# Performance work log

Hardware: AMD Instinct MI355X
Metric: run time of the kernel (lower is better)

The kernel has to match this reference:

```python
import jax, jax.numpy as jnp
import numpy as np

# Each of the 16 binary logic ops (probabilistic relaxation) is affine in (1, a, b, a*b):
# op(a,b) = c0 + ca*a + cb*b + cab*a*b. Rows indexed by op id 0..15.
COEF = jnp.array([
    [0, 0, 0, 0],   # 0: false
    [0, 0, 0, 1],   # 1: a AND b
    [0, 1, 0, -1],  # 2: a AND NOT b
    [0, 1, 0, 0],   # 3: a
    [0, 0, 1, -1],  # 4: NOT a AND b
    [0, 0, 1, 0],   # 5: b
    [0, 1, 1, -2],  # 6: a XOR b
    [0, 1, 1, -1],  # 7: a OR b
    [1, -1, -1, 1], # 8: NOR
    [1, -1, -1, 2], # 9: XNOR
    [1, 0, -1, 0],  # 10: NOT b
    [1, 0, -1, 1],  # 11: a OR NOT b
    [1, -1, 0, 0],  # 12: NOT a
    [1, -1, 0, 1],  # 13: NOT a OR b
    [1, 0, 0, -1],  # 14: NAND
    [1, 0, 0, 0],   # 15: true
], dtype=jnp.float32)

B, C, H, W = 64, 32, 32, 32
K = 64            # num_kernels
D = 4             # tree_depth
S = 2 ** D        # sample_size = 16
RF, STRIDE, PAD = 5, 1, 0


def _make_indices(rng):
    # Replicates get_kernel_indices: per-kernel random (h,w,c) offsets, tiled over all
    # spatial positions. Returns a_idx, b_idx: [K, P, S, 3] with (h, w, c).
    h_starts = np.arange(0, H + 2 * PAD - RF + 1, STRIDE)
    w_starts = np.arange(0, W + 2 * PAD - RF + 1, STRIDE)
    hg, wg = np.meshgrid(h_starts, w_starts, indexing='ij')
    hg, wg = hg.ravel(), wg.ravel()           # [P]
    a_all, b_all = [], []
    for _ in range(K):
        h_off = rng.integers(0, RF, 2 * S)
        w_off = rng.integers(0, RF, 2 * S)
        c_off = rng.integers(0, C, 2 * S)
        hh = h_off[None, :] + hg[:, None]     # [P, 2S]
        ww = w_off[None, :] + wg[:, None]
        cc = np.broadcast_to(c_off[None, :], hh.shape)
        idx = np.stack([hh, ww, cc], axis=-1) # [P, 2S, 3]
        a_all.append(idx[:, :S])
        b_all.append(idx[:, S:])
    return np.stack(a_all).astype(np.int32), np.stack(b_all).astype(np.int32)


def setup_inputs() -> dict:
    key = jax.random.key(0)
    kx, k0, k1, k2, k3, k4 = jax.random.split(key, 6)
    rng = np.random.default_rng(0)
    a_idx, b_idx = _make_indices(rng)
    return {
        'x': jax.random.uniform(kx, (B, C, H, W), dtype=jnp.float32),
        'w0': jax.random.normal(k0, (16, K, 16), dtype=jnp.float32),
        'w1': jax.random.normal(k1, (8, K, 16), dtype=jnp.float32),
        'w2': jax.random.normal(k2, (4, K, 16), dtype=jnp.float32),
        'w3': jax.random.normal(k3, (2, K, 16), dtype=jnp.float32),
        'w4': jax.random.normal(k4, (1, K, 16), dtype=jnp.float32),
        'a_idx': jnp.asarray(a_idx),
        'b_idx': jnp.asarray(b_idx),
    }


def _bin_op(a, b, w):
    # a, b: [B, K, P, L]; w: [L, K, 16] raw logits (softmaxed per original).
    p = jax.nn.softmax(w, axis=-1)                 # [L, K, 16]
    coef = jnp.einsum('lko,oc->ckl', p, COEF)      # [4, K, L]
    c = coef[:, None, :, None, :]                  # [4, 1, K, 1, L]
    return c[0] + c[1] * a + c[2] * b + c[3] * (a * b)


def reference(x, w0, w1, w2, w3, w4, a_idx, b_idx):
    ah, aw, ac = a_idx[..., 0], a_idx[..., 1], a_idx[..., 2]
    bh, bw, bc = b_idx[..., 0], b_idx[..., 1], b_idx[..., 2]
    a = x[:, ac, ah, aw]    # [B, K, P, S]
    b = x[:, bc, bh, bw]
    cur = _bin_op(a, b, w0)
    for w in (w1, w2, w3, w4):
        cur = _bin_op(cur[..., 0::2], cur[..., 1::2], w)
    return cur              # [B, K, P, 1]
```

## Files before the change

kernel.cpp:

```cpp
#include <hip/hip_runtime.h>
#include <hip/hip_bf16.h>


#define B_  64
#define C_  32
#define H_  32
#define W_  32
#define K_  64
#define P_  784
#define CHW (C_*H_*W_)
#define HW  (H_*W_)
#define SITES (K_*P_)
#define NPAIR (P_/2)

__constant__ float COEF_[16][4] = {
    {0, 0, 0, 0}, {0, 0, 0, 1}, {0, 1, 0, -1}, {0, 1, 0, 0},
    {0, 0, 1, -1}, {0, 0, 1, 0}, {0, 1, 1, -2}, {0, 1, 1, -1},
    {1, -1, -1, 1}, {1, -1, -1, 2}, {1, 0, -1, 0}, {1, 0, -1, 1},
    {1, -1, 0, 0}, {1, -1, 0, 1}, {1, 0, 0, -1}, {1, 0, 0, 0}
};

__global__ __launch_bounds__(256) void prep_kernel(
    const int* __restrict__ a_idx, const int* __restrict__ b_idx,
    const float* __restrict__ w0, const float* __restrict__ w1,
    const float* __restrict__ w2, const float* __restrict__ w3,
    const float* __restrict__ w4,
    int* __restrict__ baseAB,
    float4* __restrict__ cws)
{
    const int t = blockIdx.x * 256 + threadIdx.x;
    if (t < K_ * 32) {
        const int k = t >> 5;
        const int j = t & 31;
        const int* src = (j < 16) ? a_idx : b_idx;
        const int l = j & 15;
        const size_t ii = ((size_t)k * P_ * 16 + l) * 3;
        const int h = src[ii + 0];
        const int w = src[ii + 1];
        const int c = src[ii + 2];
        baseAB[t] = (c << 12) + (h << 7) + (w << 2);
    } else if (t < K_ * 32 + K_ * 31) {
        const int tt = t - K_ * 32;
        const int k = tt / 31;
        const int node = tt - k * 31;
        int d, l;
        if      (node < 16) { d = 0; l = node; }
        else if (node < 24) { d = 1; l = node - 16; }
        else if (node < 28) { d = 2; l = node - 24; }
        else if (node < 30) { d = 3; l = node - 28; }
        else                { d = 4; l = 0; }
        const float* W;
        switch (d) {
            case 0: W = w0; break;
            case 1: W = w1; break;
            case 2: W = w2; break;
            case 3: W = w3; break;
            default: W = w4; break;
        }
        const float* row = W + ((size_t)l * K_ + k) * 16;
        float m = row[0];
        #pragma unroll
        for (int o = 1; o < 16; ++o) m = fmaxf(m, row[o]);
        float e[16];
        float Z = 0.0f;
        #pragma unroll
        for (int o = 0; o < 16; ++o) { e[o] = expf(row[o] - m); Z += e[o]; }
        const float inv = 1.0f / Z;
        float c0 = 0.f, c1 = 0.f, c2 = 0.f, c3 = 0.f;
        #pragma unroll
        for (int o = 0; o < 16; ++o) {
            c0 += e[o] * COEF_[o][0];
            c1 += e[o] * COEF_[o][1];
            c2 += e[o] * COEF_[o][2];
            c3 += e[o] * COEF_[o][3];
        }
        cws[tt] = make_float4(c0 * inv, c1 * inv, c2 * inv, c3 * inv);
    }
}

__device__ __forceinline__ float binop(float a, float b, float4 c) {
    return fmaf(b, fmaf(c.w, a, c.z), fmaf(c.y, a, c.x));
}

__global__ __launch_bounds__(1024, 4) void logicconv_main(
    const float* __restrict__ x,
    const int* __restrict__ baseAB,
    const float4* __restrict__ cws,
    float* __restrict__ out)
{
    __shared__ float simg[CHW];

    const int tid = threadIdx.x;
    const int kg  = blockIdx.x >> 5;
    const int bp  = blockIdx.x & 31;
    const int b0  = bp * 2;

    {
        const float4* xi = (const float4*)(x + (size_t)b0 * CHW);
        float4* si = (float4*)simg;
        #pragma unroll
        for (int j = 0; j < 8; ++j)
            si[tid + j * 1024] = xi[tid + j * 1024];
    }
    __syncthreads();

    const int g    = __builtin_amdgcn_readfirstlane(tid >> 7);
    const int lane = tid & 127;
    const int k    = kg * 8 + g;

    const int*    __restrict__ bA = baseAB + k * 32;
    const float4* __restrict__ cw = cws + (size_t)k * 31;
    const char*   sb = (const char*)simg;
    const char*   x1 = (const char*)(x + (size_t)(b0 + 1) * CHW);
    float* __restrict__ o0 = out + ((size_t)b0 * K_ + k) * P_;
    float* __restrict__ o1 = o0 + (size_t)K_ * P_;

    for (int s = 0; s < 4; ++s) {
        const int t = s * 128 + lane;
        if (t < NPAIR) {
            const unsigned row  = (unsigned)t / 14u;
            const unsigned disp = 8u * (unsigned)t + 16u * row;

            float2 ye[16], yo[16];
            #pragma unroll
            for (int h = 0; h < 2; ++h) {
                unsigned ea[8], eb[8];
                #pragma unroll
                for (int j = 0; j < 8; ++j) {
                    ea[j] = (unsigned)bA[h*8 + j]      + disp;
                    eb[j] = (unsigned)bA[16 + h*8 + j] + disp;
                }
                float od[32];
                #pragma unroll
                for (int j = 0; j < 8; ++j) {
                    od[4*j+0] = *(const float*)(x1 + ea[j]);
                    od[4*j+1] = *(const float*)(x1 + ea[j] + 4);
                    od[4*j+2] = *(const float*)(x1 + eb[j]);
                    od[4*j+3] = *(const float*)(x1 + eb[j] + 4);
                }
                float ev[32];
                #pragma unroll
                for (int j = 0; j < 8; ++j) {
                    ev[4*j+0] = *(const float*)(sb + ea[j]);
                    ev[4*j+1] = *(const float*)(sb + ea[j] + 4);
                    ev[4*j+2] = *(const float*)(sb + eb[j]);
                    ev[4*j+3] = *(const float*)(sb + eb[j] + 4);
                }
                #pragma unroll
                for (int j = 0; j < 8; ++j) {
                    const int l = h*8 + j;
                    const float4 c = cw[l];
                    ye[l].x = binop(ev[4*j+0], ev[4*j+2], c);
                    ye[l].y = binop(ev[4*j+1], ev[4*j+3], c);
                    yo[l].x = binop(od[4*j+0], od[4*j+2], c);
                    yo[l].y = binop(od[4*j+1], od[4*j+3], c);
                }
            }
            #pragma unroll
            for (int l = 0; l < 8; ++l) {
                const float4 c = cw[16 + l];
                ye[l].x = binop(ye[2*l].x, ye[2*l+1].x, c);
                ye[l].y = binop(ye[2*l].y, ye[2*l+1].y, c);
                yo[l].x = binop(yo[2*l].x, yo[2*l+1].x, c);
                yo[l].y = binop(yo[2*l].y, yo[2*l+1].y, c);
            }
            #pragma unroll
            for (int l = 0; l < 4; ++l) {
                const float4 c = cw[24 + l];
                ye[l].x = binop(ye[2*l].x, ye[2*l+1].x, c);
                ye[l].y = binop(ye[2*l].y, ye[2*l+1].y, c);
                yo[l].x = binop(yo[2*l].x, yo[2*l+1].x, c);
                yo[l].y = binop(yo[2*l].y, yo[2*l+1].y, c);
            }
            #pragma unroll
            for (int l = 0; l < 2; ++l) {
                const float4 c = cw[28 + l];
                ye[l].x = binop(ye[2*l].x, ye[2*l+1].x, c);
                ye[l].y = binop(ye[2*l].y, ye[2*l+1].y, c);
                yo[l].x = binop(yo[2*l].x, yo[2*l+1].x, c);
                yo[l].y = binop(yo[2*l].y, yo[2*l+1].y, c);
            }
            {
                const float4 c = cw[30];
                float2 re, ro;
                re.x = binop(ye[0].x, ye[1].x, c);
                re.y = binop(ye[0].y, ye[1].y, c);
                ro.x = binop(yo[0].x, yo[1].x, c);
                ro.y = binop(yo[0].y, yo[1].y, c);
                *(float2*)(o0 + 2 * t) = re;
                *(float2*)(o1 + 2 * t) = ro;
            }
        }
    }
}

extern "C" void kernel_launch(void* const* d_in, const int* in_sizes, int n_in,
                              void* d_out, int out_size, void* d_ws, size_t ws_size,
                              hipStream_t stream) {
    const float* x     = (const float*)d_in[0];
    const float* w0    = (const float*)d_in[1];
    const float* w1    = (const float*)d_in[2];
    const float* w2    = (const float*)d_in[3];
    const float* w3    = (const float*)d_in[4];
    const float* w4    = (const float*)d_in[5];
    const int*   a_idx = (const int*)d_in[6];
    const int*   b_idx = (const int*)d_in[7];
    float* out = (float*)d_out;

    int*    baseAB = (int*)d_ws;
    float4* cws    = (float4*)((char*)d_ws + (size_t)K_ * 32 * 4);

    prep_kernel<<<16, 256, 0, stream>>>(a_idx, b_idx, w0, w1, w2, w3, w4,
                                        baseAB, cws);

    logicconv_main<<<256, 1024, 0, stream>>>(x, baseAB, cws, out);
}
```

Baseline: 30.15 us.

## Split shared image into even/odd columns and route some leaves to global

Stores the staged even-batch image in LDS de-interleaved into even-column and odd-column halves, with per-leaf precomputed base offsets and deltas. Each lane's stride-2 pixel pairs then map to consecutive LDS words, which aims to reduce bank conflicts. Only the first 14 leaves read from LDS. The last two leaves read directly from global memory, shifting some load from LDS onto the cache. This adds 56 registers of precomputed offsets, which may raise register pressure under the 1024-thread launch bound.

```diff
diff --git a/kernel.cpp b/kernel.cpp
--- a/kernel.cpp
+++ b/kernel.cpp
@@ -12,6 +12,7 @@
 #define HW  (H_*W_)
 #define SITES (K_*P_)
 #define NPAIR (P_/2)
+#define NLDS 14
 
 __constant__ float COEF_[16][4] = {
     {0, 0, 0, 0}, {0, 0, 0, 1}, {0, 1, 0, -1}, {0, 1, 0, 0},
@@ -97,10 +98,15 @@
 
     {
         const float4* xi = (const float4*)(x + (size_t)b0 * CHW);
-        float4* si = (float4*)simg;
-        #pragma unroll
-        for (int j = 0; j < 8; ++j)
-            si[tid + j * 1024] = xi[tid + j * 1024];
+        float2* se = (float2*)simg;
+        float2* so = ((float2*)simg) + 8192;
+        #pragma unroll
+        for (int j = 0; j < 8; ++j) {
+            const int u = tid + j * 1024;
+            const float4 v = xi[u];
+            se[u] = make_float2(v.x, v.z);
+            so[u] = make_float2(v.y, v.w);
+        }
     }
     __syncthreads();
 
@@ -110,45 +116,71 @@
 
     const int*    __restrict__ bA = baseAB + k * 32;
     const float4* __restrict__ cw = cws + (size_t)k * 31;
-    const char*   sb = (const char*)simg;
-    const char*   x1 = (const char*)(x + (size_t)(b0 + 1) * CHW);
+
+    int sB[2 * NLDS], sD[2 * NLDS];
+    #pragma unroll
+    for (int j = 0; j < NLDS; ++j) {
+        #pragma unroll
+        for (int sdx = 0; sdx < 2; ++sdx) {
+            const int bo = bA[sdx * 16 + j];
+            const int be = bo >> 2;
+            const int odd = be & 1;
+            sB[2*j + sdx] = odd ? (65536 + (((be - 1) >> 1) << 2))
+                                : ((be >> 1) << 2);
+            sD[2*j + sdx] = odd ? -65532 : 65536;
+        }
+    }
+
+    const char* sb = (const char*)simg;
+    const char* x0g = (const char*)(x + (size_t)b0 * CHW);
+    const char* x1  = (const char*)(x + (size_t)(b0 + 1) * CHW);
     float* __restrict__ o0 = out + ((size_t)b0 * K_ + k) * P_;
     float* __restrict__ o1 = o0 + (size_t)K_ * P_;
 
     for (int s = 0; s < 4; ++s) {
         const int t = s * 128 + lane;
         if (t < NPAIR) {
-            const unsigned row  = (unsigned)t / 14u;
-            const unsigned disp = 8u * (unsigned)t + 16u * row;
+            const unsigned row   = (unsigned)t / 14u;
+            const unsigned dispL = 4u * (unsigned)t + 8u * row;
+            const unsigned dispG = 8u * (unsigned)t + 16u * row;
 
             float2 ye[16], yo[16];
             #pragma unroll
             for (int h = 0; h < 2; ++h) {
-                unsigned ea[8], eb[8];
-                #pragma unroll
-                for (int j = 0; j < 8; ++j) {
-                    ea[j] = (unsigned)bA[h*8 + j]      + disp;
-                    eb[j] = (unsigned)bA[16 + h*8 + j] + disp;
-                }
                 float od[32];
                 #pragma unroll
                 for (int j = 0; j < 8; ++j) {
-                    od[4*j+0] = *(const float*)(x1 + ea[j]);
-                    od[4*j+1] = *(const float*)(x1 + ea[j] + 4);
-                    od[4*j+2] = *(const float*)(x1 + eb[j]);
-                    od[4*j+3] = *(const float*)(x1 + eb[j] + 4);
+                    const int l = h * 8 + j;
+                    const unsigned ea = (unsigned)bA[l]      + dispG;
+                    const unsigned eb = (unsigned)bA[16 + l] + dispG;
+                    od[4*j+0] = *(const float*)(x1 + ea);
+                    od[4*j+1] = *(const float*)(x1 + ea + 4);
+                    od[4*j+2] = *(const float*)(x1 + eb);
+                    od[4*j+3] = *(const float*)(x1 + eb + 4);
                 }
                 float ev[32];
                 #pragma unroll
                 for (int j = 0; j < 8; ++j) {
-                    ev[4*j+0] = *(const float*)(sb + ea[j]);
-                    ev[4*j+1] = *(const float*)(sb + ea[j] + 4);
-                    ev[4*j+2] = *(const float*)(sb + eb[j]);
-                    ev[4*j+3] = *(const float*)(sb + eb[j] + 4);
+                    const int l = h * 8 + j;
+                    if (l < NLDS) {
+                        const unsigned a0 = (unsigned)sB[2*l]     + dispL;
+                        const unsigned b0a = (unsigned)sB[2*l + 1] + dispL;
+                        ev[4*j+0] = *(const float*)(sb + a0);
+                        ev[4*j+1] = *(const float*)(sb + a0 + sD[2*l]);
+                        ev[4*j+2] = *(const float*)(sb + b0a);
+                        ev[4*j+3] = *(const float*)(sb + b0a + sD[2*l + 1]);
+                    } else {
+                        const unsigned ea = (unsigned)bA[l]      + dispG;
+                        const unsigned eb = (unsigned)bA[16 + l] + dispG;
+                        ev[4*j+0] = *(const float*)(x0g + ea);
+                        ev[4*j+1] = *(const float*)(x0g + ea + 4);
+                        ev[4*j+2] = *(const float*)(x0g + eb);
+                        ev[4*j+3] = *(const float*)(x0g + eb + 4);
+                    }
                 }
                 #pragma unroll
                 for (int j = 0; j < 8; ++j) {
-                    const int l = h*8 + j;
+                    const int l = h * 8 + j;
                     const float4 c = cw[l];
                     ye[l].x = binop(ev[4*j+0], ev[4*j+2], c);
                     ye[l].y = binop(ev[4*j+1], ev[4*j+3], c);
```

Measured after the change: 82.90 us. 175% more time.

## Split output rows into halves to shrink shared-memory image tile

Applied to the files above, without the earlier changes.

Each block now handles half of the output rows for 16 kernels instead of all rows for 8 kernels. It stages only the 18 input rows it needs per channel into shared memory (72KB instead of 128KB), using a separate channel-stride base-offset table for the local tile. The goal is to raise occupancy, with launch bounds raised to 8, and to cut the staging load. The cost is extra halo rows loaded twice across the two halves and a second index table.

```diff
diff --git a/kernel.cpp b/kernel.cpp
--- a/kernel.cpp
+++ b/kernel.cpp
@@ -11,7 +11,9 @@
 #define CHW (C_*H_*W_)
 #define HW  (H_*W_)
 #define SITES (K_*P_)
-#define NPAIR (P_/2)
+#define NPAIRH 196
+#define NROWS 18
+#define SIMGF (C_*NROWS*W_)
 
 __constant__ float COEF_[16][4] = {
     {0, 0, 0, 0}, {0, 0, 0, 1}, {0, 1, 0, -1}, {0, 1, 0, 0},
@@ -25,7 +27,8 @@
     const float* __restrict__ w0, const float* __restrict__ w1,
     const float* __restrict__ w2, const float* __restrict__ w3,
     const float* __restrict__ w4,
-    int* __restrict__ baseAB,
+    int* __restrict__ baseG,
+    int* __restrict__ baseL,
     float4* __restrict__ cws)
 {
     const int t = blockIdx.x * 256 + threadIdx.x;
@@ -38,7 +41,8 @@
         const int h = src[ii + 0];
         const int w = src[ii + 1];
         const int c = src[ii + 2];
-        baseAB[t] = (c << 12) + (h << 7) + (w << 2);
+        baseG[t] = (c << 12) + (h << 7) + (w << 2);
+        baseL[t] = (c * 2304) + (h << 7) + (w << 2);
     } else if (t < K_ * 32 + K_ * 31) {
         const int tt = t - K_ * 32;
         const int k = tt / 31;
@@ -82,73 +86,84 @@
     return fmaf(b, fmaf(c.w, a, c.z), fmaf(c.y, a, c.x));
 }
 
-__global__ __launch_bounds__(1024, 4) void logicconv_main(
+__global__ __launch_bounds__(1024, 8) void logicconv_main(
     const float* __restrict__ x,
-    const int* __restrict__ baseAB,
+    const int* __restrict__ baseG,
+    const int* __restrict__ baseL,
     const float4* __restrict__ cws,
     float* __restrict__ out)
 {
-    __shared__ float simg[CHW];
+    __shared__ float simg[SIMGF];
 
     const int tid = threadIdx.x;
-    const int kg  = blockIdx.x >> 5;
-    const int bp  = blockIdx.x & 31;
+    const int bid = blockIdx.x;
+    const int bp  = bid & 31;
+    const int ph  = (bid >> 5) & 1;
+    const int kq  = bid >> 6;
     const int b0  = bp * 2;
+    const int rlo = 14 * ph;
 
     {
-        const float4* xi = (const float4*)(x + (size_t)b0 * CHW);
+        const float4* xi = (const float4*)(x + (size_t)b0 * CHW + rlo * W_);
         float4* si = (float4*)simg;
         #pragma unroll
-        for (int j = 0; j < 8; ++j)
-            si[tid + j * 1024] = xi[tid + j * 1024];
+        for (int r = 0; r < 5; ++r) {
+            const int u = r * 1024 + tid;
+            if (u < 4608) {
+                const int c = u / 144;
+                const int j = u - c * 144;
+                si[u] = xi[c * 256 + j];
+            }
+        }
     }
     __syncthreads();
 
-    const int g    = __builtin_amdgcn_readfirstlane(tid >> 7);
-    const int lane = tid & 127;
-    const int k    = kg * 8 + g;
-
-    const int*    __restrict__ bA = baseAB + k * 32;
+    const int g    = __builtin_amdgcn_readfirstlane(tid >> 6);
+    const int lane = tid & 63;
+    const int k    = kq * 16 + g;
+
+    const int*    __restrict__ bG = baseG + k * 32;
+    const int*    __restrict__ bL = baseL + k * 32;
     const float4* __restrict__ cw = cws + (size_t)k * 31;
     const char*   sb = (const char*)simg;
-    const char*   x1 = (const char*)(x + (size_t)(b0 + 1) * CHW);
-    float* __restrict__ o0 = out + ((size_t)b0 * K_ + k) * P_;
+    const char*   x1 = (const char*)(x + (size_t)(b0 + 1) * CHW) + 1792 * ph;
+    float* __restrict__ o0 = out + ((size_t)b0 * K_ + k) * P_ + 392 * ph;
     float* __restrict__ o1 = o0 + (size_t)K_ * P_;
 
     for (int s = 0; s < 4; ++s) {
-        const int t = s * 128 + lane;
-        if (t < NPAIR) {
+        const int t = s * 64 + lane;
+        if (t < NPAIRH) {
             const unsigned row  = (unsigned)t / 14u;
             const unsigned disp = 8u * (unsigned)t + 16u * row;
 
             float2 ye[16], yo[16];
             #pragma unroll
             for (int h = 0; h < 2; ++h) {
-                unsigned ea[8], eb[8];
-                #pragma unroll
-                for (int j = 0; j < 8; ++j) {
-                    ea[j] = (unsigned)bA[h*8 + j]      + disp;
-                    eb[j] = (unsigned)bA[16 + h*8 + j] + disp;
-                }
                 float od[32];
                 #pragma unroll
                 for (int j = 0; j < 8; ++j) {
-                    od[4*j+0] = *(const float*)(x1 + ea[j]);
-                    od[4*j+1] = *(const float*)(x1 + ea[j] + 4);
-                    od[4*j+2] = *(const float*)(x1 + eb[j]);
-                    od[4*j+3] = *(const float*)(x1 + eb[j] + 4);
+                    const int l = h * 8 + j;
+                    const unsigned ga = (unsigned)bG[l]      + disp;
+                    const unsigned gb = (unsigned)bG[16 + l] + disp;
+                    od[4*j+0] = *(const float*)(x1 + ga);
+                    od[4*j+1] = *(const float*)(x1 + ga + 4);
+                    od[4*j+2] = *(const float*)(x1 + gb);
+                    od[4*j+3] = *(const float*)(x1 + gb + 4);
                 }
                 float ev[32];
                 #pragma unroll
                 for (int j = 0; j < 8; ++j) {
-                    ev[4*j+0] = *(const float*)(sb + ea[j]);
-                    ev[4*j+1] = *(const float*)(sb + ea[j] + 4);
-                    ev[4*j+2] = *(const float*)(sb + eb[j]);
-                    ev[4*j+3] = *(const float*)(sb + eb[j] + 4);
+                    const int l = h * 8 + j;
+                    const unsigned la = (unsigned)bL[l]      + disp;
+                    const unsigned lb = (unsigned)bL[16 + l] + disp;
+                    ev[4*j+0] = *(const float*)(sb + la);
+                    ev[4*j+1] = *(const float*)(sb + la + 4);
+                    ev[4*j+2] = *(const float*)(sb + lb);
+                    ev[4*j+3] = *(const float*)(sb + lb + 4);
                 }
                 #pragma unroll
                 for (int j = 0; j < 8; ++j) {
-                    const int l = h*8 + j;
+                    const int l = h * 8 + j;
                     const float4 c = cw[l];
                     ye[l].x = binop(ev[4*j+0], ev[4*j+2], c);
                     ye[l].y = binop(ev[4*j+1], ev[4*j+3], c);
@@ -207,11 +222,12 @@
     const int*   b_idx = (const int*)d_in[7];
     float* out = (float*)d_out;
 
-    int*    baseAB = (int*)d_ws;
-    float4* cws    = (float4*)((char*)d_ws + (size_t)K_ * 32 * 4);
+    int*    baseG = (int*)d_ws;
+    int*    baseL = baseG + K_ * 32;
+    float4* cws   = (float4*)(baseL + K_ * 32);
 
     prep_kernel<<<16, 256, 0, stream>>>(a_idx, b_idx, w0, w1, w2, w3, w4,
-                                        baseAB, cws);
-
-    logicconv_main<<<256, 1024, 0, stream>>>(x, baseAB, cws, out);
-}
+                                        baseG, baseL, cws);
+
+    logicconv_main<<<256, 1024, 0, stream>>>(x, baseG, baseL, cws, out);
+}
```

Result: slower. 45.84 us (+52.0%).

## Split even/odd batch images across separate waves with vectorized global gathers

Applied to the files above, without the earlier changes.

Each wave now handles a single batch image instead of every thread handling both. Half the waves read the even image from shared memory two positions at a time. The other half read the odd image straight from global memory with 16-byte loads over four adjacent positions. The tree reduction is also interleaved to shorten live ranges and cut register pressure. This separates LDS and global gather latency onto different waves, but the two halves do uneven work (7 vs 4 iterations) and the unaligned vector global loads may be slow.

```diff
diff --git a/kernel.cpp b/kernel.cpp
--- a/kernel.cpp
+++ b/kernel.cpp
@@ -12,6 +12,7 @@
 #define HW  (H_*W_)
 #define SITES (K_*P_)
 #define NPAIR (P_/2)
+#define NQUAD (P_/4)
 
 __constant__ float COEF_[16][4] = {
     {0, 0, 0, 0}, {0, 0, 0, 1}, {0, 1, 0, -1}, {0, 1, 0, 0},
@@ -19,6 +20,8 @@
     {1, -1, -1, 1}, {1, -1, -1, 2}, {1, 0, -1, 0}, {1, 0, -1, 1},
     {1, -1, 0, 0}, {1, -1, 0, 1}, {1, 0, 0, -1}, {1, 0, 0, 0}
 };
+
+typedef float f4a __attribute__((ext_vector_type(4), aligned(4)));
 
 __global__ __launch_bounds__(256) void prep_kernel(
     const int* __restrict__ a_idx, const int* __restrict__ b_idx,
@@ -104,91 +107,132 @@
     }
     __syncthreads();
 
-    const int g    = __builtin_amdgcn_readfirstlane(tid >> 7);
-    const int lane = tid & 127;
-    const int k    = kg * 8 + g;
+    const int w    = __builtin_amdgcn_readfirstlane(tid >> 6);
+    const int lane = tid & 63;
+    const int isOdd = (w >> 2) & 1;
+    const int kloc  = (w & 3) | ((w >> 3) << 2);
+    const int k     = kg * 8 + kloc;
 
     const int*    __restrict__ bA = baseAB + k * 32;
     const float4* __restrict__ cw = cws + (size_t)k * 31;
-    const char*   sb = (const char*)simg;
-    const char*   x1 = (const char*)(x + (size_t)(b0 + 1) * CHW);
-    float* __restrict__ o0 = out + ((size_t)b0 * K_ + k) * P_;
-    float* __restrict__ o1 = o0 + (size_t)K_ * P_;
-
-    for (int s = 0; s < 4; ++s) {
-        const int t = s * 128 + lane;
-        if (t < NPAIR) {
-            const unsigned row  = (unsigned)t / 14u;
-            const unsigned disp = 8u * (unsigned)t + 16u * row;
-
-            float2 ye[16], yo[16];
-            #pragma unroll
-            for (int h = 0; h < 2; ++h) {
-                unsigned ea[8], eb[8];
-                #pragma unroll
-                for (int j = 0; j < 8; ++j) {
-                    ea[j] = (unsigned)bA[h*8 + j]      + disp;
-                    eb[j] = (unsigned)bA[16 + h*8 + j] + disp;
-                }
-                float od[32];
-                #pragma unroll
-                for (int j = 0; j < 8; ++j) {
-                    od[4*j+0] = *(const float*)(x1 + ea[j]);
-                    od[4*j+1] = *(const float*)(x1 + ea[j] + 4);
-                    od[4*j+2] = *(const float*)(x1 + eb[j]);
-                    od[4*j+3] = *(const float*)(x1 + eb[j] + 4);
-                }
-                float ev[32];
-                #pragma unroll
-                for (int j = 0; j < 8; ++j) {
-                    ev[4*j+0] = *(const float*)(sb + ea[j]);
-                    ev[4*j+1] = *(const float*)(sb + ea[j] + 4);
-                    ev[4*j+2] = *(const float*)(sb + eb[j]);
-                    ev[4*j+3] = *(const float*)(sb + eb[j] + 4);
-                }
-                #pragma unroll
-                for (int j = 0; j < 8; ++j) {
-                    const int l = h*8 + j;
-                    const float4 c = cw[l];
-                    ye[l].x = binop(ev[4*j+0], ev[4*j+2], c);
-                    ye[l].y = binop(ev[4*j+1], ev[4*j+3], c);
-                    yo[l].x = binop(od[4*j+0], od[4*j+2], c);
-                    yo[l].y = binop(od[4*j+1], od[4*j+3], c);
-                }
+
+    if (!isOdd) {
+        const char* sb = (const char*)simg;
+        float* __restrict__ o0 = out + ((size_t)b0 * K_ + k) * P_;
+        for (int s = 0; s < 7; ++s) {
+            const int t = s * 64 + lane;
+            if (t < NPAIR) {
+                const unsigned row  = (unsigned)t / 14u;
+                const unsigned disp = 8u * (unsigned)t + 16u * row;
+
+                float2 y1[8];
+                #pragma unroll
+                for (int q = 0; q < 2; ++q) {
+                    float ev[32];
+                    #pragma unroll
+                    for (int j = 0; j < 8; ++j) {
+                        const int l = q * 8 + j;
+                        const unsigned la = (unsigned)bA[l]      + disp;
+                        const unsigned lb = (unsigned)bA[16 + l] + disp;
+                        ev[4*j+0] = *(const float*)(sb + la);
+                        ev[4*j+1] = *(const float*)(sb + la + 4);
+                        ev[4*j+2] = *(const float*)(sb + lb);
+                        ev[4*j+3] = *(const float*)(sb + lb + 4);
+                    }
+                    #pragma unroll
+                    for (int j = 0; j < 4; ++j) {
+                        const int l0 = q * 8 + 2 * j;
+                        const int n  = q * 4 + j;
+                        const float4 cA = cw[l0], cB = cw[l0 + 1];
+                        const float4 cL = cw[16 + n];
+                        const float z0x = binop(ev[8*j+0], ev[8*j+2], cA);
+                        const float z0y = binop(ev[8*j+1], ev[8*j+3], cA);
+                        const float z1x = binop(ev[8*j+4], ev[8*j+6], cB);
+                        const float z1y = binop(ev[8*j+5], ev[8*j+7], cB);
+                        y1[n].x = binop(z0x, z1x, cL);
+                        y1[n].y = binop(z0y, z1y, cL);
+                    }
+                }
+                float2 y2[4];
+                #pragma unroll
+                for (int l = 0; l < 4; ++l) {
+                    const float4 c = cw[24 + l];
+                    y2[l].x = binop(y1[2*l].x, y1[2*l+1].x, c);
+                    y2[l].y = binop(y1[2*l].y, y1[2*l+1].y, c);
+                }
+                float2 y3[2];
+                #pragma unroll
+                for (int l = 0; l < 2; ++l) {
+                    const float4 c = cw[28 + l];
+                    y3[l].x = binop(y2[2*l].x, y2[2*l+1].x, c);
+                    y3[l].y = binop(y2[2*l].y, y2[2*l+1].y, c);
+                }
+                const float4 c4 = cw[30];
+                float2 re;
+                re.x = binop(y3[0].x, y3[1].x, c4);
+                re.y = binop(y3[0].y, y3[1].y, c4);
+                *(float2*)(o0 + 2 * t) = re;
             }
-            #pragma unroll
-            for (int l = 0; l < 8; ++l) {
-                const float4 c = cw[16 + l];
-                ye[l].x = binop(ye[2*l].x, ye[2*l+1].x, c);
-                ye[l].y = binop(ye[2*l].y, ye[2*l+1].y, c);
-                yo[l].x = binop(yo[2*l].x, yo[2*l+1].x, c);
-                yo[l].y = binop(yo[2*l].y, yo[2*l+1].y, c);
-            }
-            #pragma unroll
-            for (int l = 0; l < 4; ++l) {
-                const float4 c = cw[24 + l];
-                ye[l].x = binop(ye[2*l].x, ye[2*l+1].x, c);
-                ye[l].y = binop(ye[2*l].y, ye[2*l+1].y, c);
-                yo[l].x = binop(yo[2*l].x, yo[2*l+1].x, c);
-                yo[l].y = binop(yo[2*l].y, yo[2*l+1].y, c);
-            }
-            #pragma unroll
-            for (int l = 0; l < 2; ++l) {
-                const float4 c = cw[28 + l];
-                ye[l].x = binop(ye[2*l].x, ye[2*l+1].x, c);
-                ye[l].y = binop(ye[2*l].y, ye[2*l+1].y, c);
-                yo[l].x = binop(yo[2*l].x, yo[2*l+1].x, c);
-                yo[l].y = binop(yo[2*l].y, yo[2*l+1].y, c);
-            }
-            {
-                const float4 c = cw[30];
-                float2 re, ro;
-                re.x = binop(ye[0].x, ye[1].x, c);
-                re.y = binop(ye[0].y, ye[1].y, c);
-                ro.x = binop(yo[0].x, yo[1].x, c);
-                ro.y = binop(yo[0].y, yo[1].y, c);
-                *(float2*)(o0 + 2 * t) = re;
-                *(float2*)(o1 + 2 * t) = ro;
+        }
+    } else {
+        const char* x1 = (const char*)(x + (size_t)(b0 + 1) * CHW);
+        float* __restrict__ o1 = out + ((size_t)(b0 + 1) * K_ + k) * P_;
+        for (int s = 0; s < 4; ++s) {
+            const int t = s * 64 + lane;
+            if (t < NQUAD) {
+                const unsigned row  = (unsigned)t / 7u;
+                const unsigned disp = 16u * (unsigned)t + 16u * row;
+
+                f4a y1[8];
+                #pragma unroll
+                for (int q = 0; q < 4; ++q) {
+                    f4a v[8];
+                    #pragma unroll
+                    for (int j = 0; j < 4; ++j) {
+                        const int l = q * 4 + j;
+                        v[2*j]   = *(const f4a*)(x1 + ((unsigned)bA[l]      + disp));
+                        v[2*j+1] = *(const f4a*)(x1 + ((unsigned)bA[16 + l] + disp));
+                    }
+                    #pragma unroll
+                    for (int j = 0; j < 2; ++j) {
+                        const int l0 = q * 4 + 2 * j;
+                        const int n  = q * 2 + j;
+                        const float4 cA = cw[l0], cB = cw[l0 + 1];
+                        const float4 cL = cw[16 + n];
+                        f4a z0, z1;
+                        #pragma unroll
+                        for (int e = 0; e < 4; ++e) {
+                            z0[e] = binop(v[4*j    ][e], v[4*j + 1][e], cA);
+                            z1[e] = binop(v[4*j + 2][e], v[4*j + 3][e], cB);
+                        }
+                        #pragma unroll
+                        for (int e = 0; e < 4; ++e)
+                            y1[n][e] = binop(z0[e], z1[e], cL);
+                    }
+                }
+                f4a y2[4];
+                #pragma unroll
+                for (int l = 0; l < 4; ++l) {
+                    const float4 c = cw[24 + l];
+                    #pragma unroll
+                    for (int e = 0; e < 4; ++e)
+                        y2[l][e] = binop(y1[2*l][e], y1[2*l+1][e], c);
+                }
+                f4a y3[2];
+                #pragma unroll
+                for (int l = 0; l < 2; ++l) {
+                    const float4 c = cw[28 + l];
+                    #pragma unroll
+                    for (int e = 0; e < 4; ++e)
+                        y3[l][e] = binop(y2[2*l][e], y2[2*l+1][e], c);
+                }
+                const float4 c4 = cw[30];
+                float4 ro;
+                ro.x = binop(y3[0][0], y3[1][0], c4);
+                ro.y = binop(y3[0][1], y3[1][1], c4);
+                ro.z = binop(y3[0][2], y3[1][2], c4);
+                ro.w = binop(y3[0][3], y3[1][3], c4);
+                *(float4*)(o1 + 4 * t) = ro;
             }
         }
     }
```

After: 28.51 us (median of 2 runs). -5.5%, faster.
